# Kernel tuning notes

Measured on AMD Instinct MI355X. Metric: run time of the kernel, lower is better.

Reference implementation:

```python
import jax, jax.numpy as jnp
import numpy as np

N_NODES = 20000
N_EDGES = 640000
F_IN = 128
HID = 128


def setup_inputs() -> dict:
    key = jax.random.key(0)
    ks = jax.random.split(key, 12)
    d = {}
    d["x"] = jax.random.normal(ks[0], (N_NODES, F_IN), dtype=jnp.float32)
    d["edge_index"] = jax.random.randint(ks[1], (2, N_EDGES), 0, N_NODES, dtype=jnp.int64)
    d["edge_weight"] = jax.random.uniform(ks[2], (N_EDGES,), dtype=jnp.float32)
    d["h"] = jax.random.normal(ks[3], (N_NODES, HID), dtype=jnp.float32)
    s1 = 1.0 / np.sqrt(F_IN)
    s2 = 1.0 / np.sqrt(HID)
    s3 = 1.0 / np.sqrt(2 * HID)
    d["W1"] = jax.random.uniform(ks[4], (F_IN, HID), jnp.float32, -s1, s1)
    d["b1"] = jnp.zeros((HID,), jnp.float32)
    d["W2"] = jax.random.uniform(ks[5], (HID, HID), jnp.float32, -s2, s2)
    d["b2"] = jnp.zeros((HID,), jnp.float32)
    d["Wu"] = jax.random.uniform(ks[6], (2 * HID, HID), jnp.float32, -s3, s3)
    d["bu"] = jax.random.uniform(ks[7], (HID,), jnp.float32, -s3, s3)
    d["Wr"] = jax.random.uniform(ks[8], (2 * HID, HID), jnp.float32, -s3, s3)
    d["br"] = jax.random.uniform(ks[9], (HID,), jnp.float32, -s3, s3)
    d["Wc"] = jax.random.uniform(ks[10], (2 * HID, HID), jnp.float32, -s3, s3)
    d["bc"] = jax.random.uniform(ks[11], (HID,), jnp.float32, -s3, s3)
    return d


def _gcn_layer(x, W, b, src, dst, norm, n):
    # GCNConv: transform then normalized scatter-add aggregation
    xw = x @ W                                    # [N, out]
    agg = jax.ops.segment_sum(xw[src] * norm[:, None], dst, num_segments=n)
    return agg + b


def reference(x, edge_index, edge_weight, h, W1, b1, W2, b2, Wu, bu, Wr, br, Wc, bc):
    n = x.shape[0]
    loops = jnp.arange(n, dtype=edge_index.dtype)
    src = jnp.concatenate([edge_index[0], loops])
    dst = jnp.concatenate([edge_index[1], loops])
    ew = jnp.concatenate([edge_weight, jnp.ones((n,), edge_weight.dtype)])
    # symmetric GCN normalization with self-loops
    deg = jax.ops.segment_sum(ew, dst, num_segments=n)
    dinv = jnp.where(deg > 0, jax.lax.rsqrt(deg), 0.0)
    norm = dinv[src] * ew * dinv[dst]             # [E+N]
    # 2-layer GCN: in->hid (ReLU) -> hid->hid
    h1 = jax.nn.relu(_gcn_layer(x, W1, b1, src, dst, norm, n))
    g = _gcn_layer(h1, W2, b2, src, dst, norm, n)
    xg = jax.nn.sigmoid(g)                        # [N, HID]
    # GRU-style gating
    xh = jnp.concatenate([xg, h], axis=-1)        # [N, 2*HID]
    u = jax.nn.sigmoid(xh @ Wu + bu)
    r = jax.nn.sigmoid(xh @ Wr + br)
    c = jnp.tanh(jnp.concatenate([xg, r * h], axis=-1) @ Wc + bc)
    return u * h + (1.0 - u) * c
```

## Files before the change

### kernel.cpp

```cpp
#include <hip/hip_runtime.h>
#include <math.h>

#define N_NODES 20000
#define N_EDGES 640000
#define HID 128
#define NPAD 20224
#define NBLK 79
#define NSHARD 8

typedef __attribute__((ext_vector_type(8))) short bf16x8;
typedef __attribute__((ext_vector_type(4))) float f32x4;
typedef __attribute__((ext_vector_type(2))) float f32x2;

#define FIX_SCALE 274877906944.0
#define FIX_MASK ((1ull << 48) - 1)

__device__ inline short f2bf(float f) {
    unsigned u = __builtin_bit_cast(unsigned, f);
    u += 0x7fffu + ((u >> 16) & 1u);
    return (short)(u >> 16);
}
__device__ inline float bf2f(short s) {
    unsigned u = ((unsigned)(unsigned short)s) << 16;
    return __builtin_bit_cast(float, u);
}
__device__ inline uint2 pack_bf4(float4 f) {
    uint2 v;
    v.x = (unsigned)(unsigned short)f2bf(f.x) | ((unsigned)(unsigned short)f2bf(f.y) << 16);
    v.y = (unsigned)(unsigned short)f2bf(f.z) | ((unsigned)(unsigned short)f2bf(f.w) << 16);
    return v;
}
__device__ inline bf16x8 cvt8(float4 a0, float4 a1) {
    bf16x8 v;
    v[0] = f2bf(a0.x); v[1] = f2bf(a0.y); v[2] = f2bf(a0.z); v[3] = f2bf(a0.w);
    v[4] = f2bf(a1.x); v[5] = f2bf(a1.y); v[6] = f2bf(a1.z); v[7] = f2bf(a1.w);
    return v;
}
__device__ inline unsigned char f2fp8(float f) {
    return (unsigned char)(__builtin_amdgcn_cvt_pk_fp8_f32(f, f, 0, false) & 0xff);
}
__device__ inline float4 unpack_fp8x4(unsigned v) {
    f32x2 lo = __builtin_amdgcn_cvt_pk_f32_fp8((int)v, false);
    f32x2 hi = __builtin_amdgcn_cvt_pk_f32_fp8((int)v, true);
    return make_float4(lo[0], lo[1], hi[0], hi[1]);
}

__device__ inline float4 agg_node(int node, int half, int l,
                                  const unsigned char* __restrict__ xw,
                                  const int* __restrict__ rp,
                                  const int2* __restrict__ csr,
                                  const float* __restrict__ dinv) {
    float4 acc = {0.f, 0.f, 0.f, 0.f};
    if (half == 0) {
        float dv = dinv[node];
        float dv2 = dv * dv;
        float4 v = unpack_fp8x4(((const unsigned*)(xw + (size_t)node * HID))[l]);
        acc.x = v.x * dv2; acc.y = v.y * dv2; acc.z = v.z * dv2; acc.w = v.w * dv2;
    }
    int j = rp[node], end = rp[node + 1];
    int n16 = (end - j) >> 4;
    if (n16 > 0) {
        int2 e[8];
#pragma unroll
        for (int i = 0; i < 8; i++) e[i] = csr[j + 2 * i + half];
        for (int b = 0; b + 1 < n16; b++) {
            unsigned v[8];
#pragma unroll
            for (int i = 0; i < 8; i++) v[i] = ((const unsigned*)(xw + (size_t)e[i].x * HID))[l];
            int2 en[8];
            int jn = j + (b + 1) * 16;
#pragma unroll
            for (int i = 0; i < 8; i++) en[i] = csr[jn + 2 * i + half];
#pragma unroll
            for (int i = 0; i < 8; i++) {
                float w = __builtin_bit_cast(float, e[i].y);
                float4 f = unpack_fp8x4(v[i]);
                acc.x += f.x * w; acc.y += f.y * w; acc.z += f.z * w; acc.w += f.w * w;
            }
#pragma unroll
            for (int i = 0; i < 8; i++) e[i] = en[i];
        }
        {
            unsigned v[8];
#pragma unroll
            for (int i = 0; i < 8; i++) v[i] = ((const unsigned*)(xw + (size_t)e[i].x * HID))[l];
#pragma unroll
            for (int i = 0; i < 8; i++) {
                float w = __builtin_bit_cast(float, e[i].y);
                float4 f = unpack_fp8x4(v[i]);
                acc.x += f.x * w; acc.y += f.y * w; acc.z += f.z * w; acc.w += f.w * w;
            }
        }
        j += n16 * 16;
    }
    if (j + 7 < end) {
        int2 e[4];
#pragma unroll
        for (int i = 0; i < 4; i++) e[i] = csr[j + 2 * i + half];
        unsigned v[4];
#pragma unroll
        for (int i = 0; i < 4; i++) v[i] = ((const unsigned*)(xw + (size_t)e[i].x * HID))[l];
#pragma unroll
        for (int i = 0; i < 4; i++) {
            float w = __builtin_bit_cast(float, e[i].y);
            float4 f = unpack_fp8x4(v[i]);
            acc.x += f.x * w; acc.y += f.y * w; acc.z += f.z * w; acc.w += f.w * w;
        }
        j += 8;
    }
    for (; j + 1 < end; j += 2) {
        int2 e0 = csr[j + half];
        float4 f = unpack_fp8x4(((const unsigned*)(xw + (size_t)e0.x * HID))[l]);
        float w0 = __builtin_bit_cast(float, e0.y);
        acc.x += f.x * w0; acc.y += f.y * w0; acc.z += f.z * w0; acc.w += f.w * w0;
    }
    if (j < end && half == 0) {
        int2 e0 = csr[j];
        float4 f = unpack_fp8x4(((const unsigned*)(xw + (size_t)e0.x * HID))[l]);
        float w0 = __builtin_bit_cast(float, e0.y);
        acc.x += f.x * w0; acc.y += f.y * w0; acc.z += f.z * w0; acc.w += f.w * w0;
    }
    acc.x += __shfl_xor(acc.x, 32);
    acc.y += __shfl_xor(acc.y, 32);
    acc.z += __shfl_xor(acc.z, 32);
    acc.w += __shfl_xor(acc.w, 32);
    return acc;
}

__global__ __launch_bounds__(256) void k_prep(const float* __restrict__ W1, const float* __restrict__ W2,
                                              const float* __restrict__ Wu, const float* __restrict__ Wr,
                                              const float* __restrict__ Wc,
                                              short* WT1, short* WT2, short* WTu, short* WTr, short* WTc,
                                              unsigned long long* packed) {
    int b = blockIdx.x;
    int tid = threadIdx.x;
    if (b < 512) {
        int i = b * 256 + tid;
        if (i < 32768) {
            const float* W = (i < 16384) ? W1 : W2;
            short* T = (i < 16384) ? WT1 : WT2;
            int j = i & 16383;
            int n = j >> 7, k = j & 127;
            T[n * 128 + k] = f2bf(W[k * 128 + n]);
        } else {
            int j = i - 32768;
            const float* W = Wu; short* T = WTu;
            if (j >= 65536)      { W = Wc; T = WTc; j -= 65536; }
            else if (j >= 32768) { W = Wr; T = WTr; j -= 32768; }
            int n = j >> 8, k = j & 255;
            T[n * 256 + k] = f2bf(W[k * 128 + n]);
        }
    } else {
        int i = (b - 512) * 256 + tid;
        if (i < NSHARD * NPAD) packed[i] = 0ull;
    }
}

__global__ __launch_bounds__(256) void k_hist_gemm(unsigned long long* packed, int* __restrict__ rank,
                                                   const int* __restrict__ dst,
                                                   const float* __restrict__ ew,
                                                   const float* __restrict__ x,
                                                   const short* __restrict__ WT1,
                                                   unsigned char* __restrict__ xw) {
    __shared__ short As[16 * 136];
    int tid = threadIdx.x;
    if (blockIdx.x < 2500) {
        int e = blockIdx.x * 256 + tid;
        int shard = blockIdx.x & (NSHARD - 1);
        int d = dst[e];
        unsigned long long add = (1ull << 48) | (unsigned long long)((double)ew[e] * FIX_SCALE);
        unsigned long long old = atomicAdd(&packed[shard * NPAD + d], add);
        rank[e] = (int)(old >> 48);
        return;
    }
    int r0 = (blockIdx.x - 2500) * 16;
    {
        int row = tid >> 4;
        int col0 = (tid & 15) * 8;
        const float* p = x + (size_t)(r0 + row) * HID + col0;
        *(bf16x8*)(&As[row * 136 + col0]) = cvt8(*(const float4*)p, *(const float4*)(p + 4));
    }
    __syncthreads();
    int wave = tid >> 6, lane = tid & 63;
    int m = lane & 15, quad = lane >> 4;
    f32x4 acc[2];
    acc[0] = (f32x4){0.f, 0.f, 0.f, 0.f};
    acc[1] = acc[0];
#pragma unroll
    for (int ks = 0; ks < 4; ks++) {
        int k0 = ks * 32 + quad * 8;
        bf16x8 a = *(const bf16x8*)(&As[m * 136 + k0]);
#pragma unroll
        for (int j = 0; j < 2; j++) {
            int n = (wave * 2 + j) * 16 + m;
            bf16x8 b = *(const bf16x8*)(WT1 + n * 128 + k0);
            acc[j] = __builtin_amdgcn_mfma_f32_16x16x32_bf16(a, b, acc[j], 0, 0, 0);
        }
    }
#pragma unroll
    for (int j = 0; j < 2; j++) {
        int col = (wave * 2 + j) * 16 + m;
#pragma unroll
        for (int rg = 0; rg < 4; rg++) {
            int grow = r0 + quad * 4 + rg;
            xw[(size_t)grow * HID + col] = f2fp8(acc[j][rg]);
        }
    }
}

__global__ __launch_bounds__(256) void k_scan_part(const unsigned long long* __restrict__ packed,
                                                   int* __restrict__ tot, int* __restrict__ bsum) {
    __shared__ int red[256];
    int tid = threadIdx.x;
    int i = blockIdx.x * 256 + tid;
    int t = 0;
    if (i < N_NODES) {
#pragma unroll
        for (int s = 0; s < NSHARD; s++) t += (int)(packed[s * NPAD + i] >> 48);
        tot[i] = t;
    }
    red[tid] = t;
    __syncthreads();
    for (int off = 128; off > 0; off >>= 1) {
        if (tid < off) red[tid] += red[tid + off];
        __syncthreads();
    }
    if (tid == 0) bsum[blockIdx.x] = red[0];
}

__global__ __launch_bounds__(256) void k_scan_final(const unsigned long long* __restrict__ packed,
                                                    const int* __restrict__ tot,
                                                    const int* __restrict__ bsum,
                                                    int* __restrict__ rp, int* __restrict__ sb,
                                                    float* __restrict__ dinv) {
    __shared__ int smem[256];
    __shared__ int red[256];
    int tid = threadIdx.x;
    red[tid] = (tid < blockIdx.x) ? bsum[tid] : 0;
    int i = blockIdx.x * 256 + tid;
    int t = (i < N_NODES) ? tot[i] : 0;
    smem[tid] = t;
    __syncthreads();
    for (int off = 128; off > 0; off >>= 1) {
        if (tid < off) red[tid] += red[tid + off];
        __syncthreads();
    }
    for (int off = 1; off < 256; off <<= 1) {
        int x = (tid >= off) ? smem[tid - off] : 0;
        __syncthreads();
        smem[tid] += x;
        __syncthreads();
    }
    if (i < N_NODES) {
        int excl = smem[tid] - t + red[0];
        rp[i] = excl;
        if (i == N_NODES - 1) rp[N_NODES] = excl + t;
        int acc = excl;
        double deg = 1.0;
#pragma unroll
        for (int s = 0; s < NSHARD; s++) {
            unsigned long long p = packed[s * NPAD + i];
            sb[s * NPAD + i] = acc;
            acc += (int)(p >> 48);
            deg += (double)(p & FIX_MASK) * (1.0 / FIX_SCALE);
        }
        dinv[i] = rsqrtf((float)deg);
    }
}

__global__ __launch_bounds__(256) void k_fill(const int* __restrict__ src,
                                              const int* __restrict__ dst,
                                              const float* __restrict__ ew,
                                              const float* __restrict__ dinv,
                                              const int* __restrict__ sb,
                                              const int* __restrict__ rank,
                                              int2* __restrict__ csr) {
    int e = blockIdx.x * 256 + threadIdx.x;
    int shard = blockIdx.x & (NSHARD - 1);
    if (e < N_EDGES) {
        int s = src[e], d = dst[e];
        int slot = sb[shard * NPAD + d] + rank[e];
        float w = dinv[s] * ew[e] * dinv[d];
        csr[slot] = make_int2(s, __builtin_bit_cast(int, w));
    }
}

__global__ __launch_bounds__(256) void k_agg(const unsigned char* __restrict__ xw,
                                             short* __restrict__ outb,
                                             const int* __restrict__ rp,
                                             const int2* __restrict__ csr,
                                             const float* __restrict__ dinv,
                                             const float* __restrict__ bias,
                                             int act) {
    int node = blockIdx.x * 4 + (threadIdx.x >> 6);
    int lane = threadIdx.x & 63;
    int half = lane >> 5, l = lane & 31;
    float4 acc = agg_node(node, half, l, xw, rp, csr, dinv);
    if (half == 0) {
        float4 b = ((const float4*)bias)[l];
        acc.x += b.x; acc.y += b.y; acc.z += b.z; acc.w += b.w;
        if (act == 0) {
            acc.x = fmaxf(acc.x, 0.f); acc.y = fmaxf(acc.y, 0.f);
            acc.z = fmaxf(acc.z, 0.f); acc.w = fmaxf(acc.w, 0.f);
        } else {
            acc.x = 1.f / (1.f + __expf(-acc.x)); acc.y = 1.f / (1.f + __expf(-acc.y));
            acc.z = 1.f / (1.f + __expf(-acc.z)); acc.w = 1.f / (1.f + __expf(-acc.w));
        }
        ((uint2*)(outb + (size_t)node * HID))[l] = pack_bf4(acc);
    }
}

__global__ __launch_bounds__(256) void k_gemm2(const short* __restrict__ Ab,
                                               const short* __restrict__ WT,
                                               unsigned char* __restrict__ Cb) {
    __shared__ short As[16 * 136];
    int tid = threadIdx.x;
    int r0 = blockIdx.x * 16;
    {
        int row = tid >> 4;
        int col0 = (tid & 15) * 8;
        *(bf16x8*)(&As[row * 136 + col0]) = *(const bf16x8*)(Ab + (size_t)(r0 + row) * HID + col0);
    }
    __syncthreads();
    int wave = tid >> 6, lane = tid & 63;
    int m = lane & 15, quad = lane >> 4;
    f32x4 acc[2];
    acc[0] = (f32x4){0.f, 0.f, 0.f, 0.f};
    acc[1] = acc[0];
#pragma unroll
    for (int ks = 0; ks < 4; ks++) {
        int k0 = ks * 32 + quad * 8;
        bf16x8 a = *(const bf16x8*)(&As[m * 136 + k0]);
#pragma unroll
        for (int j = 0; j < 2; j++) {
            int n = (wave * 2 + j) * 16 + m;
            bf16x8 b = *(const bf16x8*)(WT + n * 128 + k0);
            acc[j] = __builtin_amdgcn_mfma_f32_16x16x32_bf16(a, b, acc[j], 0, 0, 0);
        }
    }
#pragma unroll
    for (int j = 0; j < 2; j++) {
        int col = (wave * 2 + j) * 16 + m;
#pragma unroll
        for (int rg = 0; rg < 4; rg++) {
            int grow = r0 + quad * 4 + rg;
            Cb[(size_t)grow * HID + col] = f2fp8(acc[j][rg]);
        }
    }
}

__global__ __launch_bounds__(256) void k_gate(const short* __restrict__ xgb,
                                              const float* __restrict__ hf,
                                              const short* __restrict__ WTu, const short* __restrict__ WTr,
                                              const short* __restrict__ WTc,
                                              const float* __restrict__ pbu, const float* __restrict__ pbr,
                                              const float* __restrict__ pbc,
                                              float* __restrict__ out) {
    __shared__ short Xs[32 * 264];
    int tid = threadIdx.x;
    int r0 = blockIdx.x * 32;
#pragma unroll
    for (int i = 0; i < 4; i++) {
        int c = tid + i * 256;
        int row = c >> 5;
        int col0 = (c & 31) * 8;
        int grow = r0 + row;
        bf16x8 v;
        if (col0 < 128) {
            v = *(const bf16x8*)(xgb + (size_t)grow * HID + col0);
        } else {
            const float* p = hf + (size_t)grow * HID + (col0 - 128);
            v = cvt8(*(const float4*)p, *(const float4*)(p + 4));
        }
        *(bf16x8*)(&Xs[row * 264 + col0]) = v;
    }
    __syncthreads();
    int wave = tid >> 6, lane = tid & 63;
    int m = lane & 15, quad = lane >> 4;
    f32x4 au[2][2], ar[2][2];
#pragma unroll
    for (int j = 0; j < 2; j++)
#pragma unroll
        for (int rt = 0; rt < 2; rt++) { au[j][rt] = (f32x4){0.f, 0.f, 0.f, 0.f}; ar[j][rt] = au[j][rt]; }
#pragma unroll
    for (int ks = 0; ks < 8; ks++) {
        int k0 = ks * 32 + quad * 8;
        bf16x8 a0 = *(const bf16x8*)(&Xs[m * 264 + k0]);
        bf16x8 a1 = *(const bf16x8*)(&Xs[(16 + m) * 264 + k0]);
#pragma unroll
        for (int j = 0; j < 2; j++) {
            int n = (wave * 2 + j) * 16 + m;
            bf16x8 bu_f = *(const bf16x8*)(WTu + n * 256 + k0);
            au[j][0] = __builtin_amdgcn_mfma_f32_16x16x32_bf16(a0, bu_f, au[j][0], 0, 0, 0);
            au[j][1] = __builtin_amdgcn_mfma_f32_16x16x32_bf16(a1, bu_f, au[j][1], 0, 0, 0);
            bf16x8 br_f = *(const bf16x8*)(WTr + n * 256 + k0);
            ar[j][0] = __builtin_amdgcn_mfma_f32_16x16x32_bf16(a0, br_f, ar[j][0], 0, 0, 0);
            ar[j][1] = __builtin_amdgcn_mfma_f32_16x16x32_bf16(a1, br_f, ar[j][1], 0, 0, 0);
        }
    }
    __syncthreads();
#pragma unroll
    for (int j = 0; j < 2; j++) {
        int col = (wave * 2 + j) * 16 + m;
        float brv = pbr[col];
#pragma unroll
        for (int rt = 0; rt < 2; rt++) {
#pragma unroll
            for (int rg = 0; rg < 4; rg++) {
                int trow = rt * 16 + quad * 4 + rg;
                float rv = 1.f / (1.f + __expf(-(ar[j][rt][rg] + brv)));
                float hv = bf2f(Xs[trow * 264 + 128 + col]);
                Xs[trow * 264 + 128 + col] = f2bf(rv * hv);
            }
        }
    }
    __syncthreads();
    f32x4 ac[2][2];
#pragma unroll
    for (int j = 0; j < 2; j++)
#pragma unroll
        for (int rt = 0; rt < 2; rt++) ac[j][rt] = (f32x4){0.f, 0.f, 0.f, 0.f};
#pragma unroll
    for (int ks = 0; ks < 8; ks++) {
        int k0 = ks * 32 + quad * 8;
        bf16x8 a0 = *(const bf16x8*)(&Xs[m * 264 + k0]);
        bf16x8 a1 = *(const bf16x8*)(&Xs[(16 + m) * 264 + k0]);
#pragma unroll
        for (int j = 0; j < 2; j++) {
            int n = (wave * 2 + j) * 16 + m;
            bf16x8 bc_f = *(const bf16x8*)(WTc + n * 256 + k0);
            ac[j][0] = __builtin_amdgcn_mfma_f32_16x16x32_bf16(a0, bc_f, ac[j][0], 0, 0, 0);
            ac[j][1] = __builtin_amdgcn_mfma_f32_16x16x32_bf16(a1, bc_f, ac[j][1], 0, 0, 0);
        }
    }
#pragma unroll
    for (int j = 0; j < 2; j++) {
        int col = (wave * 2 + j) * 16 + m;
        float buv = pbu[col], bcv = pbc[col];
#pragma unroll
        for (int rt = 0; rt < 2; rt++) {
#pragma unroll
            for (int rg = 0; rg < 4; rg++) {
                int grow = r0 + rt * 16 + quad * 4 + rg;
                float uv = 1.f / (1.f + __expf(-(au[j][rt][rg] + buv)));
                float cv = tanhf(ac[j][rt][rg] + bcv);
                float hv = hf[(size_t)grow * HID + col];
                out[(size_t)grow * HID + col] = uv * hv + (1.f - uv) * cv;
            }
        }
    }
}

extern "C" void kernel_launch(void* const* d_in, const int* in_sizes, int n_in,
                              void* d_out, int out_size, void* d_ws, size_t ws_size,
                              hipStream_t stream) {
    const float* x  = (const float*)d_in[0];
    const int*   ei = (const int*)d_in[1];
    const float* ew = (const float*)d_in[2];
    const float* h  = (const float*)d_in[3];
    const float* W1 = (const float*)d_in[4];
    const float* b1 = (const float*)d_in[5];
    const float* W2 = (const float*)d_in[6];
    const float* b2 = (const float*)d_in[7];
    const float* Wu = (const float*)d_in[8];
    const float* bu = (const float*)d_in[9];
    const float* Wr = (const float*)d_in[10];
    const float* br = (const float*)d_in[11];
    const float* Wc = (const float*)d_in[12];
    const float* bc = (const float*)d_in[13];
    const int* src = ei;
    const int* dst = ei + N_EDGES;
    float* out = (float*)d_out;

    const size_t NH = (size_t)N_NODES * HID;
    float* ws = (float*)d_ws;
    float* dinv = ws;
    int*   rp   = (int*)(ws + NPAD);
    unsigned long long* packed = (unsigned long long*)(ws + 2 * NPAD);
    int*   sb   = (int*)(ws + 18 * NPAD);
    int*   tot  = (int*)(ws + 26 * NPAD);
    int*   bsum = (int*)(ws + 27 * NPAD);
    int*   rank = (int*)(ws + 27 * NPAD + 128);
    int2*  csr  = (int2*)(ws + 27 * NPAD + 128 + N_EDGES);
    unsigned char* xw  = (unsigned char*)(ws + 27 * NPAD + 128 + 3 * N_EDGES);
    unsigned char* xw2 = xw + NH;
    short* h1b = (short*)(xw2 + NH);
    short* xgb = h1b + NH;
    short* WT1 = xgb + NH;
    short* WT2 = WT1 + 16384;
    short* WTu = WT2 + 16384;
    short* WTr = WTu + 32768;
    short* WTc = WTr + 32768;

    k_prep<<<512 + (NSHARD * NPAD + 255) / 256, 256, 0, stream>>>(
        W1, W2, Wu, Wr, Wc, WT1, WT2, WTu, WTr, WTc, packed);
    k_hist_gemm<<<2500 + N_NODES / 16, 256, 0, stream>>>(packed, rank, dst, ew, x, WT1, xw);
    k_scan_part<<<NBLK, 256, 0, stream>>>(packed, tot, bsum);
    k_scan_final<<<NBLK, 256, 0, stream>>>(packed, tot, bsum, rp, sb, dinv);
    k_fill<<<N_EDGES / 256, 256, 0, stream>>>(src, dst, ew, dinv, sb, rank, csr);
    k_agg<<<N_NODES / 4, 256, 0, stream>>>(xw, h1b, rp, csr, dinv, b1, 0);
    k_gemm2<<<N_NODES / 16, 256, 0, stream>>>(h1b, WT2, xw2);
    k_agg<<<N_NODES / 4, 256, 0, stream>>>(xw2, xgb, rp, csr, dinv, b2, 1);
    k_gate<<<N_NODES / 32, 256, 0, stream>>>(xgb, h, WTu, WTr, WTc, bu, br, bc, out);
}
```

Measured before the change: 220.6 us.

## Merge graph-build kernels into one cooperative persistent kernel with grid syncs

Replaces the five preprocessing launches (weight prep, histogram plus first GEMM, two scan passes, CSR fill) with a single cooperative kernel of 1024 blocks. The blocks loop over the old work units and separate the phases with grid.sync(). The aim is to remove per-launch overhead and the gaps between kernels on the same stream. In exchange, each grid-wide barrier has a cost, the grid is capped at a size that can be co-resident (launch_bounds 256,4), and the scan phases run on only 79 blocks while the rest of the grid waits.

```diff
diff --git a/kernel.cpp b/kernel.cpp
--- a/kernel.cpp
+++ b/kernel.cpp
@@ -1,12 +1,13 @@
 #include <hip/hip_runtime.h>
+#include <hip/hip_cooperative_groups.h>
 #include <math.h>
 
 #define N_NODES 20000
 #define N_EDGES 640000
 #define HID 128
 #define NPAD 20224
-#define NBLK 79
 #define NSHARD 8
+#define CGRID 1024
 
 typedef __attribute__((ext_vector_type(8))) short bf16x8;
 typedef __attribute__((ext_vector_type(4))) float f32x4;
@@ -127,157 +128,149 @@
     return acc;
 }
 
-__global__ __launch_bounds__(256) void k_prep(const float* __restrict__ W1, const float* __restrict__ W2,
-                                              const float* __restrict__ Wu, const float* __restrict__ Wr,
-                                              const float* __restrict__ Wc,
-                                              short* WT1, short* WT2, short* WTu, short* WTr, short* WTc,
-                                              unsigned long long* packed) {
+__global__ __launch_bounds__(256, 4) void k_build(
+        const float* __restrict__ W1, const float* __restrict__ W2,
+        const float* __restrict__ Wu, const float* __restrict__ Wr, const float* __restrict__ Wc,
+        short* WT1, short* WT2, short* WTu, short* WTr, short* WTc,
+        unsigned long long* packed, int* rank,
+        const int* __restrict__ dst, const float* __restrict__ ew,
+        const float* __restrict__ x, unsigned char* xw,
+        int* tot, int* bsum, int* rp, int* sb, float* dinv,
+        const int* __restrict__ src, int2* csr) {
+    cooperative_groups::grid_group grid = cooperative_groups::this_grid();
+    __shared__ short As[16 * 136];
+    __shared__ int red[256];
+    __shared__ int smem2[256];
+    __shared__ int red2[256];
     int b = blockIdx.x;
     int tid = threadIdx.x;
-    if (b < 512) {
+
+    for (int u = b; u < 1144; u += CGRID) {
+        if (u < 512) {
+            int i = u * 256 + tid;
+            if (i < 32768) {
+                const float* W = (i < 16384) ? W1 : W2;
+                short* T = (i < 16384) ? WT1 : WT2;
+                int j = i & 16383;
+                int n = j >> 7, k = j & 127;
+                T[n * 128 + k] = f2bf(W[k * 128 + n]);
+            } else {
+                int j = i - 32768;
+                const float* W = Wu; short* T = WTu;
+                if (j >= 65536)      { W = Wc; T = WTc; j -= 65536; }
+                else if (j >= 32768) { W = Wr; T = WTr; j -= 32768; }
+                int n = j >> 8, k = j & 255;
+                T[n * 256 + k] = f2bf(W[k * 128 + n]);
+            }
+        } else {
+            int i = (u - 512) * 256 + tid;
+            if (i < NSHARD * NPAD) packed[i] = 0ull;
+        }
+    }
+    grid.sync();
+
+    for (int u = b; u < 3750; u += CGRID) {
+        if (u < 2500) {
+            int e = u * 256 + tid;
+            int shard = u & (NSHARD - 1);
+            int d = dst[e];
+            unsigned long long add = (1ull << 48) | (unsigned long long)((double)ew[e] * FIX_SCALE);
+            unsigned long long old = atomicAdd(&packed[shard * NPAD + d], add);
+            rank[e] = (int)(old >> 48);
+        } else {
+            int r0 = (u - 2500) * 16;
+            {
+                int row = tid >> 4;
+                int col0 = (tid & 15) * 8;
+                const float* p = x + (size_t)(r0 + row) * HID + col0;
+                *(bf16x8*)(&As[row * 136 + col0]) = cvt8(*(const float4*)p, *(const float4*)(p + 4));
+            }
+            __syncthreads();
+            int wave = tid >> 6, lane = tid & 63;
+            int m = lane & 15, quad = lane >> 4;
+            f32x4 acc[2];
+            acc[0] = (f32x4){0.f, 0.f, 0.f, 0.f};
+            acc[1] = acc[0];
+#pragma unroll
+            for (int ks = 0; ks < 4; ks++) {
+                int k0 = ks * 32 + quad * 8;
+                bf16x8 a = *(const bf16x8*)(&As[m * 136 + k0]);
+#pragma unroll
+                for (int j = 0; j < 2; j++) {
+                    int n = (wave * 2 + j) * 16 + m;
+                    bf16x8 bw = *(const bf16x8*)(WT1 + n * 128 + k0);
+                    acc[j] = __builtin_amdgcn_mfma_f32_16x16x32_bf16(a, bw, acc[j], 0, 0, 0);
+                }
+            }
+#pragma unroll
+            for (int j = 0; j < 2; j++) {
+                int col = (wave * 2 + j) * 16 + m;
+#pragma unroll
+                for (int rg = 0; rg < 4; rg++) {
+                    int grow = r0 + quad * 4 + rg;
+                    xw[(size_t)grow * HID + col] = f2fp8(acc[j][rg]);
+                }
+            }
+            __syncthreads();
+        }
+    }
+    grid.sync();
+
+    if (b < 79) {
         int i = b * 256 + tid;
-        if (i < 32768) {
-            const float* W = (i < 16384) ? W1 : W2;
-            short* T = (i < 16384) ? WT1 : WT2;
-            int j = i & 16383;
-            int n = j >> 7, k = j & 127;
-            T[n * 128 + k] = f2bf(W[k * 128 + n]);
-        } else {
-            int j = i - 32768;
-            const float* W = Wu; short* T = WTu;
-            if (j >= 65536)      { W = Wc; T = WTc; j -= 65536; }
-            else if (j >= 32768) { W = Wr; T = WTr; j -= 32768; }
-            int n = j >> 8, k = j & 255;
-            T[n * 256 + k] = f2bf(W[k * 128 + n]);
-        }
-    } else {
-        int i = (b - 512) * 256 + tid;
-        if (i < NSHARD * NPAD) packed[i] = 0ull;
-    }
-}
-
-__global__ __launch_bounds__(256) void k_hist_gemm(unsigned long long* packed, int* __restrict__ rank,
-                                                   const int* __restrict__ dst,
-                                                   const float* __restrict__ ew,
-                                                   const float* __restrict__ x,
-                                                   const short* __restrict__ WT1,
-                                                   unsigned char* __restrict__ xw) {
-    __shared__ short As[16 * 136];
-    int tid = threadIdx.x;
-    if (blockIdx.x < 2500) {
-        int e = blockIdx.x * 256 + tid;
-        int shard = blockIdx.x & (NSHARD - 1);
-        int d = dst[e];
-        unsigned long long add = (1ull << 48) | (unsigned long long)((double)ew[e] * FIX_SCALE);
-        unsigned long long old = atomicAdd(&packed[shard * NPAD + d], add);
-        rank[e] = (int)(old >> 48);
-        return;
-    }
-    int r0 = (blockIdx.x - 2500) * 16;
-    {
-        int row = tid >> 4;
-        int col0 = (tid & 15) * 8;
-        const float* p = x + (size_t)(r0 + row) * HID + col0;
-        *(bf16x8*)(&As[row * 136 + col0]) = cvt8(*(const float4*)p, *(const float4*)(p + 4));
-    }
-    __syncthreads();
-    int wave = tid >> 6, lane = tid & 63;
-    int m = lane & 15, quad = lane >> 4;
-    f32x4 acc[2];
-    acc[0] = (f32x4){0.f, 0.f, 0.f, 0.f};
-    acc[1] = acc[0];
-#pragma unroll
-    for (int ks = 0; ks < 4; ks++) {
-        int k0 = ks * 32 + quad * 8;
-        bf16x8 a = *(const bf16x8*)(&As[m * 136 + k0]);
-#pragma unroll
-        for (int j = 0; j < 2; j++) {
-            int n = (wave * 2 + j) * 16 + m;
-            bf16x8 b = *(const bf16x8*)(WT1 + n * 128 + k0);
-            acc[j] = __builtin_amdgcn_mfma_f32_16x16x32_bf16(a, b, acc[j], 0, 0, 0);
-        }
-    }
-#pragma unroll
-    for (int j = 0; j < 2; j++) {
-        int col = (wave * 2 + j) * 16 + m;
-#pragma unroll
-        for (int rg = 0; rg < 4; rg++) {
-            int grow = r0 + quad * 4 + rg;
-            xw[(size_t)grow * HID + col] = f2fp8(acc[j][rg]);
-        }
-    }
-}
-
-__global__ __launch_bounds__(256) void k_scan_part(const unsigned long long* __restrict__ packed,
-                                                   int* __restrict__ tot, int* __restrict__ bsum) {
-    __shared__ int red[256];
-    int tid = threadIdx.x;
-    int i = blockIdx.x * 256 + tid;
-    int t = 0;
-    if (i < N_NODES) {
-#pragma unroll
-        for (int s = 0; s < NSHARD; s++) t += (int)(packed[s * NPAD + i] >> 48);
-        tot[i] = t;
-    }
-    red[tid] = t;
-    __syncthreads();
-    for (int off = 128; off > 0; off >>= 1) {
-        if (tid < off) red[tid] += red[tid + off];
+        int t = 0;
+        if (i < N_NODES) {
+#pragma unroll
+            for (int s = 0; s < NSHARD; s++) t += (int)(packed[s * NPAD + i] >> 48);
+            tot[i] = t;
+        }
+        red[tid] = t;
         __syncthreads();
-    }
-    if (tid == 0) bsum[blockIdx.x] = red[0];
-}
-
-__global__ __launch_bounds__(256) void k_scan_final(const unsigned long long* __restrict__ packed,
-                                                    const int* __restrict__ tot,
-                                                    const int* __restrict__ bsum,
-                                                    int* __restrict__ rp, int* __restrict__ sb,
-                                                    float* __restrict__ dinv) {
-    __shared__ int smem[256];
-    __shared__ int red[256];
-    int tid = threadIdx.x;
-    red[tid] = (tid < blockIdx.x) ? bsum[tid] : 0;
-    int i = blockIdx.x * 256 + tid;
-    int t = (i < N_NODES) ? tot[i] : 0;
-    smem[tid] = t;
-    __syncthreads();
-    for (int off = 128; off > 0; off >>= 1) {
-        if (tid < off) red[tid] += red[tid + off];
+        for (int off = 128; off > 0; off >>= 1) {
+            if (tid < off) red[tid] += red[tid + off];
+            __syncthreads();
+        }
+        if (tid == 0) bsum[b] = red[0];
+    }
+    grid.sync();
+
+    if (b < 79) {
+        red2[tid] = (tid < b) ? bsum[tid] : 0;
+        int i = b * 256 + tid;
+        int t = (i < N_NODES) ? tot[i] : 0;
+        smem2[tid] = t;
         __syncthreads();
-    }
-    for (int off = 1; off < 256; off <<= 1) {
-        int x = (tid >= off) ? smem[tid - off] : 0;
-        __syncthreads();
-        smem[tid] += x;
-        __syncthreads();
-    }
-    if (i < N_NODES) {
-        int excl = smem[tid] - t + red[0];
-        rp[i] = excl;
-        if (i == N_NODES - 1) rp[N_NODES] = excl + t;
-        int acc = excl;
-        double deg = 1.0;
-#pragma unroll
-        for (int s = 0; s < NSHARD; s++) {
-            unsigned long long p = packed[s * NPAD + i];
-            sb[s * NPAD + i] = acc;
-            acc += (int)(p >> 48);
-            deg += (double)(p & FIX_MASK) * (1.0 / FIX_SCALE);
-        }
-        dinv[i] = rsqrtf((float)deg);
-    }
-}
-
-__global__ __launch_bounds__(256) void k_fill(const int* __restrict__ src,
-                                              const int* __restrict__ dst,
-                                              const float* __restrict__ ew,
-                                              const float* __restrict__ dinv,
-                                              const int* __restrict__ sb,
-                                              const int* __restrict__ rank,
-                                              int2* __restrict__ csr) {
-    int e = blockIdx.x * 256 + threadIdx.x;
-    int shard = blockIdx.x & (NSHARD - 1);
-    if (e < N_EDGES) {
+        for (int off = 128; off > 0; off >>= 1) {
+            if (tid < off) red2[tid] += red2[tid + off];
+            __syncthreads();
+        }
+        for (int off = 1; off < 256; off <<= 1) {
+            int xv = (tid >= off) ? smem2[tid - off] : 0;
+            __syncthreads();
+            smem2[tid] += xv;
+            __syncthreads();
+        }
+        if (i < N_NODES) {
+            int excl = smem2[tid] - t + red2[0];
+            rp[i] = excl;
+            if (i == N_NODES - 1) rp[N_NODES] = excl + t;
+            int acc = excl;
+            double deg = 1.0;
+#pragma unroll
+            for (int s = 0; s < NSHARD; s++) {
+                unsigned long long p = packed[s * NPAD + i];
+                sb[s * NPAD + i] = acc;
+                acc += (int)(p >> 48);
+                deg += (double)(p & FIX_MASK) * (1.0 / FIX_SCALE);
+            }
+            dinv[i] = rsqrtf((float)deg);
+        }
+    }
+    grid.sync();
+
+    for (int u = b; u < 2500; u += CGRID) {
+        int e = u * 256 + tid;
+        int shard = u & (NSHARD - 1);
         int s = src[e], d = dst[e];
         int slot = sb[shard * NPAD + d] + rank[e];
         float w = dinv[s] * ew[e] * dinv[d];
@@ -492,12 +485,16 @@
     short* WTr = WTu + 32768;
     short* WTc = WTr + 32768;
 
-    k_prep<<<512 + (NSHARD * NPAD + 255) / 256, 256, 0, stream>>>(
-        W1, W2, Wu, Wr, Wc, WT1, WT2, WTu, WTr, WTc, packed);
-    k_hist_gemm<<<2500 + N_NODES / 16, 256, 0, stream>>>(packed, rank, dst, ew, x, WT1, xw);
-    k_scan_part<<<NBLK, 256, 0, stream>>>(packed, tot, bsum);
-    k_scan_final<<<NBLK, 256, 0, stream>>>(packed, tot, bsum, rp, sb, dinv);
-    k_fill<<<N_EDGES / 256, 256, 0, stream>>>(src, dst, ew, dinv, sb, rank, csr);
+    void* args[] = {
+        (void*)&W1, (void*)&W2, (void*)&Wu, (void*)&Wr, (void*)&Wc,
+        (void*)&WT1, (void*)&WT2, (void*)&WTu, (void*)&WTr, (void*)&WTc,
+        (void*)&packed, (void*)&rank, (void*)&dst, (void*)&ew,
+        (void*)&x, (void*)&xw,
+        (void*)&tot, (void*)&bsum, (void*)&rp, (void*)&sb, (void*)&dinv,
+        (void*)&src, (void*)&csr
+    };
+    hipLaunchCooperativeKernel((void*)k_build, dim3(CGRID), dim3(256), args, 0, stream);
+
     k_agg<<<N_NODES / 4, 256, 0, stream>>>(xw, h1b, rp, csr, dinv, b1, 0);
     k_gemm2<<<N_NODES / 16, 256, 0, stream>>>(h1b, WT2, xw2);
     k_agg<<<N_NODES / 4, 256, 0, stream>>>(xw2, xgb, rp, csr, dinv, b2, 1);
```

Result: slower. 684.7 us (+210.4%).
